# Optimization experiments

Hardware: AMD Instinct MI355X
Metric: run time of the kernel (lower is better)

Reference implementation:

```python
import jax, jax.numpy as jnp
import numpy as np

EMB_DIM = 256
HEAD_DIM = 32


def setup_inputs() -> dict:
    key = jax.random.key(0)
    kx, kq, kk, kv = jax.random.split(key, 4)
    B, S = 4, 4096
    x = jax.random.normal(kx, (B, S, EMB_DIM), dtype=jnp.float32)
    # Linear(emb_dim, head_dim, bias=False): store as [emb_dim, head_dim]
    sc = 1.0 / np.sqrt(EMB_DIM)
    Wq = jax.random.normal(kq, (EMB_DIM, HEAD_DIM), dtype=jnp.float32) * sc
    Wk = jax.random.normal(kk, (EMB_DIM, HEAD_DIM), dtype=jnp.float32) * sc
    Wv = jax.random.normal(kv, (EMB_DIM, HEAD_DIM), dtype=jnp.float32) * sc
    return {"x": x, "Wq": Wq, "Wk": Wk, "Wv": Wv}


def reference(x, Wq, Wk, Wv):
    # single-head attention with POST-softmax scaling (as in source).
    # Dropout treated as identity (eval mode) for determinism.
    scaling = HEAD_DIM ** (-0.5)
    q = jnp.einsum('bse,ed->bsd', x, Wq)
    k = jnp.einsum('bse,ed->bsd', x, Wk)
    v = jnp.einsum('bse,ed->bsd', x, Wv)
    energy = jnp.einsum('bqd,bkd->bqk', q, k)  # [B,S,S]
    att = jax.nn.softmax(energy, axis=-1) * scaling
    out = jnp.einsum('bqk,bkd->bqd', att, v)
    return out
```

## Files before the change

### kernel.cpp

```cpp
#include <hip/hip_runtime.h>

#define EMB 256
#define HD 32
#define SEQ 4096
#define NSPLIT 16
#define KRANGE 256
#define NQROW 16384

typedef _Float16 half8 __attribute__((ext_vector_type(8)));
typedef _Float16 half4v __attribute__((ext_vector_type(4)));
typedef float floatx4 __attribute__((ext_vector_type(4)));
typedef float floatx16 __attribute__((ext_vector_type(16)));

#define L2E 1.44269504088896340736f
#define SCALING 0.17677669529663687f

__device__ __forceinline__ half8 mk8(unsigned a, unsigned b, unsigned c, unsigned d) {
  union { unsigned u[4]; half8 h; } z;
  z.u[0] = a; z.u[1] = b; z.u[2] = c; z.u[3] = d;
  return z.h;
}

__global__ __launch_bounds__(256) void prep_kernel(const float* __restrict__ Wq,
                                                   const float* __restrict__ Wk,
                                                   const float* __restrict__ Wv,
                                                   _Float16* __restrict__ wsw) {
  int gid = blockIdx.x * 256 + threadIdx.x;
  int j    = gid & 7;
  int lane = (gid >> 3) & 63;
  int kc   = (gid >> 9) & 7;
  int half = (gid >> 12) & 1;
  int mat  = gid >> 13;
  const float* W = (mat == 0) ? Wq : ((mat == 1) ? Wk : Wv);
  int n = lane & 15, quad = lane >> 4;
  int e = kc * 32 + quad * 8 + j;
  int d = n + half * 16;
  float v = W[e * HD + d];
  if (mat == 0) v *= L2E;
  wsw[gid] = (_Float16)v;
}

__global__ __launch_bounds__(256) void qkv_kernel(const float* __restrict__ x,
                                                  const _Float16* __restrict__ wsw,
                                                  _Float16* __restrict__ qw,
                                                  _Float16* __restrict__ kw,
                                                  _Float16* __restrict__ vt2) {
  int lane = threadIdx.x & 63, wave = threadIdx.x >> 6;
  int n = lane & 15, quad = lane >> 4;
  int mat = blockIdx.y;
  int rowbase = blockIdx.x * 64 + wave * 16;

  floatx4 c0 = {0,0,0,0}, c1 = {0,0,0,0};

#pragma unroll
  for (int kc = 0; kc < 8; ++kc) {
    const float* xp = x + (rowbase + n) * EMB + kc * 32 + quad * 8;
    float4 xa = *(const float4*)(xp);
    float4 xb = *(const float4*)(xp + 4);
    half8 a;
    a[0] = (_Float16)xa.x; a[1] = (_Float16)xa.y; a[2] = (_Float16)xa.z; a[3] = (_Float16)xa.w;
    a[4] = (_Float16)xb.x; a[5] = (_Float16)xb.y; a[6] = (_Float16)xb.z; a[7] = (_Float16)xb.w;
    half8 b0 = *(const half8*)(wsw + (((mat * 2 + 0) * 8 + kc) << 9) + (lane << 3));
    half8 b1 = *(const half8*)(wsw + (((mat * 2 + 1) * 8 + kc) << 9) + (lane << 3));
    c0 = __builtin_amdgcn_mfma_f32_16x16x32_f16(a, b0, c0, 0, 0, 0);
    c1 = __builtin_amdgcn_mfma_f32_16x16x32_f16(a, b1, c1, 0, 0, 0);
  }

  if (mat == 2) {
    int b = rowbase >> 12;
    int s0 = rowbase & (SEQ - 1);
    _Float16* vb = vt2 + (size_t)b * SEQ * HD;
#pragma unroll
    for (int r = 0; r < 4; ++r) {
      int s = s0 + quad * 4 + r;
      int blk = (s >> 3) << 8, sl = s & 7;
      vb[blk + n * 8 + sl]        = (_Float16)c0[r];
      vb[blk + (n + 16) * 8 + sl] = (_Float16)c1[r];
    }
  } else {
    _Float16* dst = (mat == 0) ? qw : kw;
#pragma unroll
    for (int r = 0; r < 4; ++r) {
      int row = rowbase + quad * 4 + r;
      dst[row * HD + n]      = (_Float16)c0[r];
      dst[row * HD + n + 16] = (_Float16)c1[r];
    }
  }
}

__global__ __launch_bounds__(256, 4) void attn_kernel(const _Float16* __restrict__ q,
                                                      const _Float16* __restrict__ k,
                                                      const _Float16* __restrict__ vt2,
                                                      _Float16* __restrict__ Op,
                                                      float* __restrict__ Mp,
                                                      float* __restrict__ Lp) {
  const int t = threadIdx.x;
  const int w = t >> 6, lane = t & 63;
  const int n2 = lane & 31, h = lane >> 5;
  const int qb = blockIdx.x & 127;
  const int sp = blockIdx.x >> 7;
  const int b = qb >> 5;
  const int qrow0 = qb * 128 + w * 32;
  const int key0 = sp * KRANGE;

  const _Float16* kb = k   + (size_t)(b * SEQ + key0) * HD;
  const _Float16* vb = vt2 + (size_t)b * SEQ * HD + (size_t)key0 * HD;

  half8 qb0 = *(const half8*)(q + (qrow0 + n2) * HD + h * 8);
  half8 qb1 = *(const half8*)(q + (qrow0 + n2) * HD + 16 + h * 8);

  floatx16 o;
#pragma unroll
  for (int r = 0; r < 16; ++r) o[r] = 0.f;
  const floatx16 zero16 = o;
  float m = -__builtin_huge_valf();
  float l = 0.f;

  half8 ka0 = *(const half8*)(kb + (size_t)n2 * HD + h * 8);
  half8 ka1 = *(const half8*)(kb + (size_t)n2 * HD + 16 + h * 8);
  half8 va0 = *(const half8*)(vb + h * 256 + n2 * 8);
  half8 va1 = *(const half8*)(vb + 512 + h * 256 + n2 * 8);

#pragma unroll
  for (int kt = 0; kt < KRANGE / 32; ++kt) {
    half8 nka0, nka1, nva0, nva1;
    if (kt + 1 < KRANGE / 32) {
      const _Float16* kn = kb + (size_t)((kt + 1) * 32 + n2) * HD;
      const _Float16* vn = vb + (kt + 1) * 1024;
      nka0 = *(const half8*)(kn + h * 8);
      nka1 = *(const half8*)(kn + 16 + h * 8);
      nva0 = *(const half8*)(vn + h * 256 + n2 * 8);
      nva1 = *(const half8*)(vn + 512 + h * 256 + n2 * 8);
    }

    floatx16 s = __builtin_amdgcn_mfma_f32_32x32x16_f16(ka0, qb0, zero16, 0, 0, 0);
    s = __builtin_amdgcn_mfma_f32_32x32x16_f16(ka1, qb1, s, 0, 0, 0);

    floatx4 s0 = {s[0], s[1], s[2], s[3]};
    floatx4 s1 = {s[4], s[5], s[6], s[7]};
    floatx4 s2 = {s[8], s[9], s[10], s[11]};
    floatx4 s3 = {s[12], s[13], s[14], s[15]};
    floatx4 t01 = __builtin_elementwise_max(s0, s1);
    floatx4 t23 = __builtin_elementwise_max(s2, s3);
    floatx4 t4  = __builtin_elementwise_max(t01, t23);
    float mm = fmaxf(fmaxf(t4[0], t4[1]), fmaxf(t4[2], t4[3]));
    mm = fmaxf(mm, __shfl_xor(mm, 32));
    float mnew = fmaxf(m, mm);
    float alpha = __builtin_amdgcn_exp2f(m - mnew);
    m = mnew;

    float p[16];
#pragma unroll
    for (int r = 0; r < 16; ++r) p[r] = __builtin_amdgcn_exp2f(s[r] - mnew);
    unsigned pk[8];
#pragma unroll
    for (int g = 0; g < 8; ++g)
      pk[g] = __builtin_bit_cast(unsigned, __builtin_amdgcn_cvt_pkrtz(p[2 * g], p[2 * g + 1]));

    float ps = ((p[0] + p[1]) + (p[2] + p[3])) + ((p[4] + p[5]) + (p[6] + p[7]))
             + ((p[8] + p[9]) + (p[10] + p[11])) + ((p[12] + p[13]) + (p[14] + p[15]));
    ps += __shfl_xor(ps, 32);
    l = l * alpha + ps;

#pragma unroll
    for (int r = 0; r < 16; ++r) o[r] *= alpha;

    unsigned tmp0 = h ? pk[0] : pk[2];
    unsigned tmp1 = h ? pk[1] : pk[3];
    unsigned tmp2 = h ? pk[4] : pk[6];
    unsigned tmp3 = h ? pk[5] : pk[7];
    unsigned ex0 = (unsigned)__shfl_xor((int)tmp0, 32);
    unsigned ex1 = (unsigned)__shfl_xor((int)tmp1, 32);
    unsigned ex2 = (unsigned)__shfl_xor((int)tmp2, 32);
    unsigned ex3 = (unsigned)__shfl_xor((int)tmp3, 32);
    half8 B0 = h ? mk8(ex0, ex1, pk[2], pk[3]) : mk8(pk[0], pk[1], ex0, ex1);
    half8 B1 = h ? mk8(ex2, ex3, pk[6], pk[7]) : mk8(pk[4], pk[5], ex2, ex3);

    o = __builtin_amdgcn_mfma_f32_32x32x16_f16(va0, B0, o, 0, 0, 0);
    o = __builtin_amdgcn_mfma_f32_32x32x16_f16(va1, B1, o, 0, 0, 0);

    ka0 = nka0; ka1 = nka1; va0 = nva0; va1 = nva1;
  }

  size_t obase = ((size_t)(sp * NQROW + qrow0) + n2) * 32;
#pragma unroll
  for (int bb = 0; bb < 4; ++bb) {
    half4v pv;
    pv[0] = (_Float16)o[4 * bb + 0];
    pv[1] = (_Float16)o[4 * bb + 1];
    pv[2] = (_Float16)o[4 * bb + 2];
    pv[3] = (_Float16)o[4 * bb + 3];
    *(half4v*)&Op[obase + 8 * bb + 4 * h] = pv;
  }
  if (h == 0) {
    int mi = sp * NQROW + qrow0 + n2;
    Mp[mi] = m;
    Lp[mi] = l;
  }
}

__global__ __launch_bounds__(256) void combine_kernel(const _Float16* __restrict__ Op,
                                                      const float* __restrict__ Mp,
                                                      const float* __restrict__ Lp,
                                                      float* __restrict__ out) {
  int gid = blockIdx.x * 256 + threadIdx.x;
  int dc = gid & 7, qrow = gid >> 3;
  float mv[NSPLIT];
  float ms = -__builtin_huge_valf();
#pragma unroll
  for (int sp = 0; sp < NSPLIT; ++sp) {
    mv[sp] = Mp[sp * NQROW + qrow];
    ms = fmaxf(ms, mv[sp]);
  }
  float L = 0.f;
  floatx4 O = {0.f, 0.f, 0.f, 0.f};
#pragma unroll
  for (int sp = 0; sp < NSPLIT; ++sp) {
    float ww = __builtin_amdgcn_exp2f(mv[sp] - ms);
    L += ww * Lp[sp * NQROW + qrow];
    half4v ov = *(const half4v*)&Op[((size_t)(sp * NQROW + qrow)) * 32 + dc * 4];
#pragma unroll
    for (int r = 0; r < 4; ++r) O[r] += ww * (float)ov[r];
  }
  float inv = SCALING / L;
  floatx4 res = {O[0] * inv, O[1] * inv, O[2] * inv, O[3] * inv};
  *(floatx4*)&out[qrow * HD + dc * 4] = res;
}

extern "C" void kernel_launch(void* const* d_in, const int* in_sizes, int n_in,
                              void* d_out, int out_size, void* d_ws, size_t ws_size,
                              hipStream_t stream) {
  const float* x  = (const float*)d_in[0];
  const float* Wq = (const float*)d_in[1];
  const float* Wk = (const float*)d_in[2];
  const float* Wv = (const float*)d_in[3];
  float* out = (float*)d_out;

  _Float16* wsw = (_Float16*)d_ws;
  _Float16* qw  = wsw + 24576;
  _Float16* kw  = qw + NQROW * HD;
  _Float16* vt2 = kw + NQROW * HD;
  _Float16* Op  = vt2 + NQROW * HD;
  float* Mp = (float*)(Op + (size_t)NSPLIT * NQROW * 32);
  float* Lp = Mp + NSPLIT * NQROW;

  prep_kernel<<<96, 256, 0, stream>>>(Wq, Wk, Wv, wsw);
  qkv_kernel<<<dim3(256, 3), 256, 0, stream>>>(x, wsw, qw, kw, vt2);
  attn_kernel<<<2048, 256, 0, stream>>>(qw, kw, vt2, Op, Mp, Lp);
  combine_kernel<<<512, 256, 0, stream>>>(Op, Mp, Lp, out);
}
```

Before: 99.59 us.

## Pre-tile K into MFMA fragment layout and halve the attention key split count

The QKV projection now writes K in a tiled layout that matches the MFMA operand fragment order, so each lane loads contiguous 16-byte chunks (lane*8) instead of strided row reads. The split-K factor drops from 16 to 8 with 512 keys per block, halving the attention grid and the partial outputs the combine kernel must merge. The loop unroll is reduced to 2. The trade is less parallelism (1024 blocks) against fewer partials and more coalesced K loads, and the combine kernel must agree with the new NSPLIT.

```diff
diff --git a/kernel.cpp b/kernel.cpp
--- a/kernel.cpp
+++ b/kernel.cpp
@@ -3,8 +3,8 @@
 #define EMB 256
 #define HD 32
 #define SEQ 4096
-#define NSPLIT 16
-#define KRANGE 256
+#define NSPLIT 8
+#define KRANGE 512
 #define NQROW 16384
 
 typedef _Float16 half8 __attribute__((ext_vector_type(8)));
@@ -43,7 +43,7 @@
 __global__ __launch_bounds__(256) void qkv_kernel(const float* __restrict__ x,
                                                   const _Float16* __restrict__ wsw,
                                                   _Float16* __restrict__ qw,
-                                                  _Float16* __restrict__ kw,
+                                                  _Float16* __restrict__ kt2,
                                                   _Float16* __restrict__ vt2) {
   int lane = threadIdx.x & 63, wave = threadIdx.x >> 6;
   int n = lane & 15, quad = lane >> 4;
@@ -66,7 +66,26 @@
     c1 = __builtin_amdgcn_mfma_f32_16x16x32_f16(a, b1, c1, 0, 0, 0);
   }
 
-  if (mat == 2) {
+  if (mat == 0) {
+#pragma unroll
+    for (int r = 0; r < 4; ++r) {
+      int row = rowbase + quad * 4 + r;
+      qw[row * HD + n]      = (_Float16)c0[r];
+      qw[row * HD + n + 16] = (_Float16)c1[r];
+    }
+  } else if (mat == 1) {
+    int b = rowbase >> 12;
+    int s0 = rowbase & (SEQ - 1);
+    _Float16* kb2 = kt2 + (size_t)b * SEQ * HD;
+    int hi = (n >> 3) << 5, j = n & 7;
+#pragma unroll
+    for (int r = 0; r < 4; ++r) {
+      int s = s0 + quad * 4 + r;
+      int tb = (s >> 5) << 10, n2k = s & 31;
+      kb2[tb + ((n2k + hi) << 3) + j]       = (_Float16)c0[r];
+      kb2[tb + 512 + ((n2k + hi) << 3) + j] = (_Float16)c1[r];
+    }
+  } else {
     int b = rowbase >> 12;
     int s0 = rowbase & (SEQ - 1);
     _Float16* vb = vt2 + (size_t)b * SEQ * HD;
@@ -77,19 +96,11 @@
       vb[blk + n * 8 + sl]        = (_Float16)c0[r];
       vb[blk + (n + 16) * 8 + sl] = (_Float16)c1[r];
     }
-  } else {
-    _Float16* dst = (mat == 0) ? qw : kw;
-#pragma unroll
-    for (int r = 0; r < 4; ++r) {
-      int row = rowbase + quad * 4 + r;
-      dst[row * HD + n]      = (_Float16)c0[r];
-      dst[row * HD + n + 16] = (_Float16)c1[r];
-    }
   }
 }
 
 __global__ __launch_bounds__(256, 4) void attn_kernel(const _Float16* __restrict__ q,
-                                                      const _Float16* __restrict__ k,
+                                                      const _Float16* __restrict__ kt2,
                                                       const _Float16* __restrict__ vt2,
                                                       _Float16* __restrict__ Op,
                                                       float* __restrict__ Mp,
@@ -103,8 +114,8 @@
   const int qrow0 = qb * 128 + w * 32;
   const int key0 = sp * KRANGE;
 
-  const _Float16* kb = k   + (size_t)(b * SEQ + key0) * HD;
-  const _Float16* vb = vt2 + (size_t)b * SEQ * HD + (size_t)key0 * HD;
+  const _Float16* kb = kt2 + (size_t)(b * SEQ + key0) * HD;
+  const _Float16* vb = vt2 + (size_t)(b * SEQ + key0) * HD;
 
   half8 qb0 = *(const half8*)(q + (qrow0 + n2) * HD + h * 8);
   half8 qb1 = *(const half8*)(q + (qrow0 + n2) * HD + 16 + h * 8);
@@ -116,21 +127,21 @@
   float m = -__builtin_huge_valf();
   float l = 0.f;
 
-  half8 ka0 = *(const half8*)(kb + (size_t)n2 * HD + h * 8);
-  half8 ka1 = *(const half8*)(kb + (size_t)n2 * HD + 16 + h * 8);
-  half8 va0 = *(const half8*)(vb + h * 256 + n2 * 8);
-  half8 va1 = *(const half8*)(vb + 512 + h * 256 + n2 * 8);
-
-#pragma unroll
+  half8 ka0 = *(const half8*)(kb + lane * 8);
+  half8 ka1 = *(const half8*)(kb + 512 + lane * 8);
+  half8 va0 = *(const half8*)(vb + lane * 8);
+  half8 va1 = *(const half8*)(vb + 512 + lane * 8);
+
+#pragma unroll 2
   for (int kt = 0; kt < KRANGE / 32; ++kt) {
     half8 nka0, nka1, nva0, nva1;
     if (kt + 1 < KRANGE / 32) {
-      const _Float16* kn = kb + (size_t)((kt + 1) * 32 + n2) * HD;
+      const _Float16* kn = kb + (kt + 1) * 1024;
       const _Float16* vn = vb + (kt + 1) * 1024;
-      nka0 = *(const half8*)(kn + h * 8);
-      nka1 = *(const half8*)(kn + 16 + h * 8);
-      nva0 = *(const half8*)(vn + h * 256 + n2 * 8);
-      nva1 = *(const half8*)(vn + 512 + h * 256 + n2 * 8);
+      nka0 = *(const half8*)(kn + lane * 8);
+      nka1 = *(const half8*)(kn + 512 + lane * 8);
+      nva0 = *(const half8*)(vn + lane * 8);
+      nva1 = *(const half8*)(vn + 512 + lane * 8);
     }
 
     floatx16 s = __builtin_amdgcn_mfma_f32_32x32x16_f16(ka0, qb0, zero16, 0, 0, 0);
@@ -238,14 +249,14 @@
 
   _Float16* wsw = (_Float16*)d_ws;
   _Float16* qw  = wsw + 24576;
-  _Float16* kw  = qw + NQROW * HD;
-  _Float16* vt2 = kw + NQROW * HD;
+  _Float16* kt2 = qw + NQROW * HD;
+  _Float16* vt2 = kt2 + NQROW * HD;
   _Float16* Op  = vt2 + NQROW * HD;
   float* Mp = (float*)(Op + (size_t)NSPLIT * NQROW * 32);
   float* Lp = Mp + NSPLIT * NQROW;
 
   prep_kernel<<<96, 256, 0, stream>>>(Wq, Wk, Wv, wsw);
-  qkv_kernel<<<dim3(256, 3), 256, 0, stream>>>(x, wsw, qw, kw, vt2);
-  attn_kernel<<<2048, 256, 0, stream>>>(qw, kw, vt2, Op, Mp, Lp);
+  qkv_kernel<<<dim3(256, 3), 256, 0, stream>>>(x, wsw, qw, kt2, vt2);
+  attn_kernel<<<1024, 256, 0, stream>>>(qw, kt2, vt2, Op, Mp, Lp);
   combine_kernel<<<512, 256, 0, stream>>>(Op, Mp, Lp, out);
 }
```

After: 100.6 us. No clear change (+1.0%).
